# Kernel optimization log

Measured on AMD Instinct MI355X. Metric: run time of the kernel, lower is better.

## Reference

```python
import jax, jax.numpy as jnp
import numpy as np

B, NS, NQ = 128, 128, 512
D_IN, D_OUT = 256, 64


def setup_inputs() -> dict:
    key = jax.random.key(0)
    ks = jax.random.split(key, 6)
    return {
        "phi_support": jax.random.normal(ks[0], (B, NS, D_IN), dtype=jnp.float32),
        "y_support": jax.random.normal(ks[1], (B, NS, D_OUT), dtype=jnp.float32),
        "phi_query": jax.random.normal(ks[2], (B, NQ, D_IN), dtype=jnp.float32),
        "y_query": jax.random.normal(ks[3], (B, NQ, D_OUT), dtype=jnp.float32),
        # xavier-uniform-ish params
        "m_prior": jax.random.uniform(ks[4], (D_IN, D_OUT), minval=-1.0, maxval=1.0) * np.sqrt(6.0 / (D_IN + D_OUT)),
        "S_inv_prior_asym": jax.random.uniform(ks[5], (D_IN, D_IN), minval=-1.0, maxval=1.0) * np.sqrt(6.0 / (2 * D_IN)),
        "sig_eps": jnp.array([0.1], dtype=jnp.float32),
    }


def reference(phi_support, y_support, phi_query, y_query, m_prior, S_inv_prior_asym, sig_eps):
    alpha = 1.0
    d_out = m_prior.shape[1]
    # prior precision (symmetric PSD by construction) and natural-param prior mean
    S_inv_prior = alpha * (S_inv_prior_asym @ S_inv_prior_asym.T)          # [D_in, D_in]
    m_prior_nat = S_inv_prior @ m_prior                                     # [D_in, D_out]
    # posterior precision / covariance per task (nobs > 0 branch)
    S_inv = jnp.einsum('bni,bnj->bij', phi_support, phi_support) + S_inv_prior  # [B, D_in, D_in]
    S = jnp.linalg.inv(S_inv)                                               # batched small inverse
    rhs = jnp.einsum('bni,bnk->bik', phi_support, y_support) + m_prior_nat  # [B, D_in, D_out]
    m = S @ rhs                                                             # [B, D_in, D_out]
    # predictive mean and spread
    mu = phi_query @ m                                                      # [B, Q, D_out]
    spread_fac = 1.0 + jnp.einsum('bqi,bij,bqj->bq', phi_query, S, phi_query)  # [B, Q]
    # sig = spread_fac (x) (eye * sig_eps) : diagonal [B, Q, D_out, D_out]
    diag = jnp.eye(d_out, dtype=mu.dtype) * sig_eps                         # [D_out, D_out]
    sig = spread_fac[..., None, None] * diag
    # nll: logdet of diagonal sig + quadratic form with its inverse (diag -> reciprocal)
    logdet = d_out * (jnp.log(spread_fac) + jnp.log(sig_eps))               # [B, Q]
    resid = y_query - mu
    quadf = jnp.sum(resid * resid, axis=-1) / (spread_fac * sig_eps)        # [B, Q]
    nll = logdet.mean() + quadf.mean()
    return mu, sig, nll
```

## Files before the change

kernel.cpp:

```cpp
#include <hip/hip_runtime.h>
#include <math.h>

#define B_T   128
#define NS    128
#define NQ    512
#define DIN   256
#define DOUT  64

#define MU_SIZE  (B_T*NQ*DOUT)
#define SIG_SIZE (B_T*NQ*DOUT*DOUT)
#define NLL_IDX  (MU_SIZE + SIG_SIZE)

__global__ __launch_bounds__(256) void k_prior_sp(const float* __restrict__ A,
                                                  double* __restrict__ Sp,
                                                  double* __restrict__ NLLACC) {
    __shared__ float Ai[16][260];
    __shared__ float Aj[16][260];
    int bi = blockIdx.x;
    int i0 = (bi >> 4) << 4;
    int j0 = (bi & 15) << 4;
    int tid = threadIdx.x;
    if (bi == 0 && tid == 0) NLLACC[0] = 0.0;
    for (int idx = tid; idx < 16 * 256; idx += 256) {
        int r = idx >> 8, c = idx & 255;
        Ai[r][c] = A[(i0 + r) * 256 + c];
        Aj[r][c] = A[(j0 + r) * 256 + c];
    }
    __syncthreads();
    int r = tid >> 4, c = tid & 15;
    double acc = 0.0;
    for (int k = 0; k < 256; ++k)
        acc += (double)Ai[r][k] * (double)Aj[c][k];
    Sp[(i0 + r) * 256 + (j0 + c)] = acc;
}

__global__ __launch_bounds__(256) void k_build_G(const float* __restrict__ PHI,
                                                 const double* __restrict__ Sp,
                                                 double* __restrict__ G) {
    __shared__ float As[128][64];
    __shared__ float Bs[128][64];
    int b = blockIdx.x;
    int by = blockIdx.y;
    int ti = 0;
    while (((ti + 1) * (ti + 2)) / 2 <= by) ti++;
    int tj = by - (ti * (ti + 1)) / 2;
    int i0 = ti * 64, j0 = tj * 64;
    int tid = threadIdx.x;
    const float* Pb = PHI + b * (NS * DIN);
    for (int idx = tid; idx < 128 * 64; idx += 256) {
        int n = idx >> 6, c = idx & 63;
        As[n][c] = Pb[n * 256 + i0 + c];
        Bs[n][c] = Pb[n * 256 + j0 + c];
    }
    __syncthreads();
    int tx = tid & 15, ty = tid >> 4;
    double acc[4][4];
#pragma unroll
    for (int r = 0; r < 4; ++r)
#pragma unroll
        for (int s = 0; s < 4; ++s) acc[r][s] = 0.0;
    for (int n = 0; n < 128; ++n) {
        float a0 = As[n][4 * ty + 0], a1 = As[n][4 * ty + 1];
        float a2 = As[n][4 * ty + 2], a3 = As[n][4 * ty + 3];
        float b0 = Bs[n][4 * tx + 0], b1 = Bs[n][4 * tx + 1];
        float b2 = Bs[n][4 * tx + 2], b3 = Bs[n][4 * tx + 3];
        acc[0][0] += (double)a0 * b0; acc[0][1] += (double)a0 * b1;
        acc[0][2] += (double)a0 * b2; acc[0][3] += (double)a0 * b3;
        acc[1][0] += (double)a1 * b0; acc[1][1] += (double)a1 * b1;
        acc[1][2] += (double)a1 * b2; acc[1][3] += (double)a1 * b3;
        acc[2][0] += (double)a2 * b0; acc[2][1] += (double)a2 * b1;
        acc[2][2] += (double)a2 * b2; acc[2][3] += (double)a2 * b3;
        acc[3][0] += (double)a3 * b0; acc[3][1] += (double)a3 * b1;
        acc[3][2] += (double)a3 * b2; acc[3][3] += (double)a3 * b3;
    }
    double* Gb = G + b * 65536;
#pragma unroll
    for (int r = 0; r < 4; ++r) {
        int i = i0 + 4 * ty + r;
#pragma unroll
        for (int s = 0; s < 4; ++s) {
            int j = j0 + 4 * tx + s;
            Gb[i * 256 + j] = acc[r][s] + Sp[i * 256 + j];
        }
    }
}

__global__ __launch_bounds__(256) void k_build_rhs(const float* __restrict__ PHI,
                                                   const float* __restrict__ Y,
                                                   const float* __restrict__ MP,
                                                   const double* __restrict__ Sp,
                                                   double* __restrict__ RHS,
                                                   double* __restrict__ MPNo) {
    int b = blockIdx.x, by = blockIdx.y, tid = threadIdx.x;
    if (by == 4) {
        if (b >= 4) return;
        for (int out = tid; out < 4096; out += 256) {
            int r = 64 * b + (out >> 6), cc = out & 63;
            double acc = 0.0;
            for (int t = 0; t < 256; ++t)
                acc += Sp[r * 256 + t] * (double)MP[t * 64 + cc];
            MPNo[r * 64 + cc] = acc;
        }
        return;
    }
    __shared__ float As[128][64];
    __shared__ float Ys[128][64];
    int i0 = by * 64;
    const float* Pb = PHI + b * (NS * DIN);
    const float* Yb = Y + b * (NS * DOUT);
    for (int idx = tid; idx < 128 * 64; idx += 256) {
        int n = idx >> 6, c = idx & 63;
        As[n][c] = Pb[n * 256 + i0 + c];
        Ys[n][c] = Yb[n * 64 + c];
    }
    __syncthreads();
    int tx = tid & 15, ty = tid >> 4;
    double acc[4][4];
#pragma unroll
    for (int r = 0; r < 4; ++r)
#pragma unroll
        for (int s = 0; s < 4; ++s) acc[r][s] = 0.0;
    for (int n = 0; n < 128; ++n) {
        float a0 = As[n][4 * ty + 0], a1 = As[n][4 * ty + 1];
        float a2 = As[n][4 * ty + 2], a3 = As[n][4 * ty + 3];
        float y0 = Ys[n][4 * tx + 0], y1 = Ys[n][4 * tx + 1];
        float y2 = Ys[n][4 * tx + 2], y3 = Ys[n][4 * tx + 3];
        acc[0][0] += (double)a0 * y0; acc[0][1] += (double)a0 * y1;
        acc[0][2] += (double)a0 * y2; acc[0][3] += (double)a0 * y3;
        acc[1][0] += (double)a1 * y0; acc[1][1] += (double)a1 * y1;
        acc[1][2] += (double)a1 * y2; acc[1][3] += (double)a1 * y3;
        acc[2][0] += (double)a2 * y0; acc[2][1] += (double)a2 * y1;
        acc[2][2] += (double)a2 * y2; acc[2][3] += (double)a2 * y3;
        acc[3][0] += (double)a3 * y0; acc[3][1] += (double)a3 * y1;
        acc[3][2] += (double)a3 * y2; acc[3][3] += (double)a3 * y3;
    }
    double* Rb = RHS + b * 16384;
#pragma unroll
    for (int r = 0; r < 4; ++r) {
        int i = i0 + 4 * ty + r;
#pragma unroll
        for (int s = 0; s < 4; ++s)
            Rb[i * 64 + 4 * tx + s] = acc[r][s];
    }
}

__global__ __launch_bounds__(256) void k_cholinv(double* __restrict__ G,
                                                 double* __restrict__ LT,
                                                 double* __restrict__ TI,
                                                 float* __restrict__ TIF) {
    __shared__ double S[8256];
    int b = blockIdx.x, tid = threadIdx.x;
    double* Gb = G + b * 65536;
    double* LTb = LT + b * 65536;
    double* TIb = TI + b * 65536;
    float* TIFb = TIF + b * 65536;

    double* P = S;
#define PCH(p, r) P[(p) * 258 + (r)]
    for (int k0 = 0; k0 < 256; k0 += 32) {
        int rows = 256 - k0;
        for (int idx = tid; idx < rows * 32; idx += 256) {
            int r = k0 + (idx >> 5), p = idx & 31;
            PCH(p, r) = Gb[r * 256 + k0 + p];
        }
        __syncthreads();
        for (int p = 0; p < 32; ++p) {
            int k = k0 + p;
            if (tid >= k) {
                double v = PCH(p, tid);
                for (int p2 = 0; p2 < p; ++p2) v -= PCH(p2, tid) * PCH(p2, k);
                PCH(p, tid) = v;
            }
            __syncthreads();
            double d = sqrt(fmax(PCH(p, k), 1e-300));
            double inv = 1.0 / d;
            if (tid > k) PCH(p, tid) *= inv;
            else if (tid == k) PCH(p, tid) = d;
            __syncthreads();
        }
        for (int p = 0; p < 32; ++p) {
            int k = k0 + p;
            if (tid >= k) LTb[k * 256 + tid] = PCH(p, tid);
        }
        int ty = tid >> 4, tx = tid & 15;
        for (int i2 = k0 + 32 + 2 * ty; i2 < 256; i2 += 32) {
            double pa[32], pb[32];
#pragma unroll
            for (int p = 0; p < 32; ++p) { pa[p] = PCH(p, i2); pb[p] = PCH(p, i2 + 1); }
            for (int j2 = k0 + 32 + 2 * tx; j2 <= i2 + 1; j2 += 32) {
                double g00 = 0.0, g01 = 0.0, g10 = 0.0, g11 = 0.0;
#pragma unroll
                for (int p = 0; p < 32; ++p) {
                    double q0 = PCH(p, j2), q1 = PCH(p, j2 + 1);
                    g00 += pa[p] * q0; g01 += pa[p] * q1;
                    g10 += pb[p] * q0; g11 += pb[p] * q1;
                }
                if (j2 <= i2)     Gb[i2 * 256 + j2]           -= g00;
                if (j2 + 1 <= i2) Gb[i2 * 256 + j2 + 1]       -= g01;
                Gb[(i2 + 1) * 256 + j2] -= g10;
                if (j2 <= i2)     Gb[(i2 + 1) * 256 + j2 + 1] -= g11;
            }
        }
        __syncthreads();
    }
#undef PCH

    double* SHD = S;
    for (int idx = tid; idx < 65536; idx += 256) {
        int i = idx >> 8, k = idx & 255;
        if (k > i) { TIb[idx] = 0.0; TIFb[idx] = 0.0f; }
    }
    for (int idx = tid; idx < 8192; idx += 256) {
        int g = idx >> 10, rem = idx & 1023, k = rem >> 5, i = rem & 31;
        SHD[idx] = LTb[(32 * g + k) * 256 + 32 * g + i];
    }
    __syncthreads();
    {
        int g = tid >> 5, j = tid & 31;
        const double* D = SHD + g * 1024;
        double x[32];
#pragma unroll
        for (int i = 0; i < 32; ++i) {
            double s = (i == j) ? 1.0 : 0.0;
#pragma unroll
            for (int k = 0; k < i; ++k) {
                double lv = D[k * 32 + i];
                s -= (k >= j) ? lv * x[k] : 0.0;
            }
            double inv = 1.0 / D[i * 32 + i];
            x[i] = (i >= j) ? s * inv : 0.0;
        }
#pragma unroll
        for (int i = 0; i < 32; ++i) {
            int gi = 32 * g + i, gj = 32 * g + j;
            TIb[gi * 256 + gj] = x[i];
            TIFb[gi * 256 + gj] = (float)x[i];
        }
    }
    __syncthreads();
    double* Bsh = SHD;
    int j = tid & 31, ig = tid >> 5;
    for (int I = 1; I < 8; ++I) {
        for (int J = I - 1; J >= 0; --J) {
            double acc[4] = {0.0, 0.0, 0.0, 0.0};
            for (int K = J; K < I; ++K) {
                for (int kk = 0; kk < 32; ++kk) {
                    double tv = TIb[(32 * K + kk) * 256 + 32 * J + j];
#pragma unroll
                    for (int r = 0; r < 4; ++r) {
                        double lv = LTb[(32 * K + kk) * 256 + 32 * I + ig * 4 + r];
                        acc[r] += lv * tv;
                    }
                }
            }
            __syncthreads();
#pragma unroll
            for (int r = 0; r < 4; ++r) Bsh[(ig * 4 + r) * 32 + j] = acc[r];
            __syncthreads();
            double c[4] = {0.0, 0.0, 0.0, 0.0};
            for (int k = 0; k < 32; ++k) {
                double bv = Bsh[k * 32 + j];
#pragma unroll
                for (int r = 0; r < 4; ++r) {
                    double dv = TIb[(32 * I + ig * 4 + r) * 256 + 32 * I + k];
                    c[r] -= dv * bv;
                }
            }
#pragma unroll
            for (int r = 0; r < 4; ++r) {
                int gi = 32 * I + ig * 4 + r, gj = 32 * J + j;
                TIb[gi * 256 + gj] = c[r];
                TIFb[gi * 256 + gj] = (float)c[r];
            }
        }
        __syncthreads();
    }
}

__global__ __launch_bounds__(256) void k_gemm_Z(const double* __restrict__ TI,
                                                const double* __restrict__ RHS,
                                                const double* __restrict__ MPN,
                                                double* __restrict__ Z) {
    __shared__ double As[32][64];
    __shared__ double Bs[64][64];
    int b = blockIdx.x, i0 = blockIdx.y * 32;
    int tid = threadIdx.x, c = tid & 63, rg = tid >> 6;
    const double* TIb = TI + b * 65536;
    const double* Rb = RHS + b * 16384;
    double* Zb = Z + b * 16384;
    double acc[8] = {};
    for (int k0 = 0; k0 <= i0; k0 += 64) {
        for (int idx = tid; idx < 2048; idx += 256) {
            int r = idx >> 6, kk = idx & 63;
            As[r][kk] = TIb[(i0 + r) * 256 + k0 + kk];
        }
        for (int idx = tid; idx < 4096; idx += 256) {
            int kk = idx >> 6, cc = idx & 63;
            Bs[kk][cc] = Rb[(k0 + kk) * 64 + cc] + MPN[(k0 + kk) * 64 + cc];
        }
        __syncthreads();
        for (int kk = 0; kk < 64; ++kk) {
            double bv = Bs[kk][c];
#pragma unroll
            for (int r = 0; r < 8; ++r)
                acc[r] += As[rg * 8 + r][kk] * bv;
        }
        __syncthreads();
    }
#pragma unroll
    for (int r = 0; r < 8; ++r)
        Zb[(i0 + rg * 8 + r) * 64 + c] = acc[r];
}

__global__ __launch_bounds__(256) void k_gemm_M(const double* __restrict__ TI,
                                                const double* __restrict__ Z,
                                                double* __restrict__ M) {
    __shared__ double As[64][32];
    __shared__ double Bs[64][64];
    int b = blockIdx.x, i0 = blockIdx.y * 32;
    int tid = threadIdx.x, c = tid & 63, rg = tid >> 6;
    const double* TIb = TI + b * 65536;
    const double* Zb = Z + b * 16384;
    double* Mb = M + b * 16384;
    double acc[8] = {};
    for (int k0 = (i0 >> 6) << 6; k0 < 256; k0 += 64) {
        for (int idx = tid; idx < 2048; idx += 256) {
            int kk = idx >> 5, ri = idx & 31;
            As[kk][ri] = TIb[(k0 + kk) * 256 + i0 + ri];
        }
        for (int idx = tid; idx < 4096; idx += 256) {
            int kk = idx >> 6, cc = idx & 63;
            Bs[kk][cc] = Zb[(k0 + kk) * 64 + cc];
        }
        __syncthreads();
        for (int kk = 0; kk < 64; ++kk) {
            double bv = Bs[kk][c];
#pragma unroll
            for (int r = 0; r < 8; ++r)
                acc[r] += As[kk][rg * 8 + r] * bv;
        }
        __syncthreads();
    }
#pragma unroll
    for (int r = 0; r < 8; ++r)
        Mb[(i0 + rg * 8 + r) * 64 + c] = acc[r];
}

__global__ __launch_bounds__(256) void k_spread_gemm(const float* __restrict__ PHIQ,
                                                     const float* __restrict__ TIF,
                                                     float* __restrict__ PSUM) {
    __shared__ float Qs[64][65];
    __shared__ float Ts[64][65];
    int b = blockIdx.x, q0 = blockIdx.y * 64, I = blockIdx.z, i0 = I * 64;
    int tid = threadIdx.x, tx = tid & 15, ty = tid >> 4;
    const float* Qb = PHIQ + b * (NQ * DIN) + q0 * DIN;
    const float* Tb = TIF + b * 65536;
    float acc[4][4];
#pragma unroll
    for (int r = 0; r < 4; ++r)
#pragma unroll
        for (int s = 0; s < 4; ++s) acc[r][s] = 0.0f;
    for (int k0 = 0; k0 <= i0; k0 += 64) {
        for (int idx = tid; idx < 4096; idx += 256) {
            int r = idx >> 6, c = idx & 63;
            Qs[r][c] = Qb[r * 256 + k0 + c];
            Ts[c][r] = Tb[(i0 + r) * 256 + k0 + c];
        }
        __syncthreads();
        for (int kk = 0; kk < 64; ++kk) {
            float a0 = Qs[4 * ty + 0][kk], a1 = Qs[4 * ty + 1][kk];
            float a2 = Qs[4 * ty + 2][kk], a3 = Qs[4 * ty + 3][kk];
            float b0 = Ts[kk][4 * tx + 0], b1 = Ts[kk][4 * tx + 1];
            float b2 = Ts[kk][4 * tx + 2], b3 = Ts[kk][4 * tx + 3];
            acc[0][0] += a0 * b0; acc[0][1] += a0 * b1; acc[0][2] += a0 * b2; acc[0][3] += a0 * b3;
            acc[1][0] += a1 * b0; acc[1][1] += a1 * b1; acc[1][2] += a1 * b2; acc[1][3] += a1 * b3;
            acc[2][0] += a2 * b0; acc[2][1] += a2 * b1; acc[2][2] += a2 * b2; acc[2][3] += a2 * b3;
            acc[3][0] += a3 * b0; acc[3][1] += a3 * b1; acc[3][2] += a3 * b2; acc[3][3] += a3 * b3;
        }
        __syncthreads();
    }
#pragma unroll
    for (int r = 0; r < 4; ++r) {
        float p = acc[r][0] * acc[r][0] + acc[r][1] * acc[r][1]
                + acc[r][2] * acc[r][2] + acc[r][3] * acc[r][3];
        p += __shfl_down(p, 8, 16);
        p += __shfl_down(p, 4, 16);
        p += __shfl_down(p, 2, 16);
        p += __shfl_down(p, 1, 16);
        if (tx == 0) PSUM[(size_t)(b * 4 + I) * 512 + q0 + 4 * ty + r] = p;
    }
}

__global__ __launch_bounds__(256) void k_mu_nll(const float* __restrict__ PHIQ,
                                                const double* __restrict__ M,
                                                const float* __restrict__ YQ,
                                                const float* __restrict__ PSUM,
                                                const float* __restrict__ SE,
                                                float* __restrict__ SPREAD,
                                                double* __restrict__ NLLACC,
                                                float* __restrict__ MU) {
    __shared__ float Qs[64][65];
    __shared__ float Ms[64][64];
    __shared__ double nred[64];
    int b = blockIdx.x, q0 = blockIdx.y * 64, tid = threadIdx.x;
    int tx = tid & 15, ty = tid >> 4;
    const float* Qb = PHIQ + b * (NQ * DIN) + q0 * DIN;
    const double* Mb = M + b * 16384;
    float acc[4][4];
#pragma unroll
    for (int r = 0; r < 4; ++r)
#pragma unroll
        for (int s = 0; s < 4; ++s) acc[r][s] = 0.0f;
    for (int c0 = 0; c0 < 256; c0 += 64) {
        for (int idx = tid; idx < 4096; idx += 256) {
            int r = idx >> 6, c = idx & 63;
            Qs[r][c] = Qb[r * 256 + c0 + c];
            Ms[r][c] = (float)Mb[(c0 + r) * 64 + c];
        }
        __syncthreads();
        for (int kk = 0; kk < 64; ++kk) {
            float a0 = Qs[4 * ty + 0][kk], a1 = Qs[4 * ty + 1][kk];
            float a2 = Qs[4 * ty + 2][kk], a3 = Qs[4 * ty + 3][kk];
            float b0 = Ms[kk][4 * tx + 0], b1 = Ms[kk][4 * tx + 1];
            float b2 = Ms[kk][4 * tx + 2], b3 = Ms[kk][4 * tx + 3];
            acc[0][0] += a0 * b0; acc[0][1] += a0 * b1; acc[0][2] += a0 * b2; acc[0][3] += a0 * b3;
            acc[1][0] += a1 * b0; acc[1][1] += a1 * b1; acc[1][2] += a1 * b2; acc[1][3] += a1 * b3;
            acc[2][0] += a2 * b0; acc[2][1] += a2 * b1; acc[2][2] += a2 * b2; acc[2][3] += a2 * b3;
            acc[3][0] += a3 * b0; acc[3][1] += a3 * b1; acc[3][2] += a3 * b2; acc[3][3] += a3 * b3;
        }
        __syncthreads();
    }
    float se = SE[0];
#pragma unroll
    for (int r = 0; r < 4; ++r) {
        int q = q0 + 4 * ty + r;
        float4 v = make_float4(acc[r][0], acc[r][1], acc[r][2], acc[r][3]);
        *(float4*)&MU[((size_t)b * NQ + q) * 64 + 4 * tx] = v;
        float4 y = *(const float4*)&YQ[((size_t)b * NQ + q) * 64 + 4 * tx];
        float dx = y.x - v.x, dy = y.y - v.y, dz = y.z - v.z, dw = y.w - v.w;
        float qs = dx * dx + dy * dy + dz * dz + dw * dw;
        qs += __shfl_down(qs, 8, 16);
        qs += __shfl_down(qs, 4, 16);
        qs += __shfl_down(qs, 2, 16);
        qs += __shfl_down(qs, 1, 16);
        if (tx == 0) {
            float sp = 1.0f + PSUM[(size_t)(b * 4 + 0) * 512 + q]
                            + PSUM[(size_t)(b * 4 + 1) * 512 + q]
                            + PSUM[(size_t)(b * 4 + 2) * 512 + q]
                            + PSUM[(size_t)(b * 4 + 3) * 512 + q];
            SPREAD[b * 512 + q] = sp;
            float val = 64.0f * (logf(sp) + logf(se)) + qs / (sp * se);
            nred[ty * 4 + r] = (double)val;
        }
    }
    __syncthreads();
    for (int s = 32; s > 0; s >>= 1) {
        if (tid < s) nred[tid] += nred[tid + s];
        __syncthreads();
    }
    if (tid == 0) atomicAdd(NLLACC, nred[0] * (1.0 / 65536.0));
}

__global__ __launch_bounds__(256) void k_sig(const float* __restrict__ SPREAD,
                                             const float* __restrict__ SE,
                                             const double* __restrict__ NLLACC,
                                             float* __restrict__ out) {
    __shared__ float sv_s;
    int bq = blockIdx.x, tid = threadIdx.x;
    if (bq == 0 && tid == 0) out[NLL_IDX] = (float)NLLACC[0];
    if (tid == 0) sv_s = SPREAD[bq] * SE[0];
    __syncthreads();
    float sv = sv_s;
    float* base = out + (size_t)MU_SIZE + (size_t)bq * 4096;
    int i = tid >> 2;
    int jb = (tid & 3) << 4;
    int d = i - jb;
    float vals[16];
#pragma unroll
    for (int t = 0; t < 16; ++t) vals[t] = (t == d) ? sv : 0.0f;
    float4* p = (float4*)(base + tid * 16);
    p[0] = make_float4(vals[0], vals[1], vals[2], vals[3]);
    p[1] = make_float4(vals[4], vals[5], vals[6], vals[7]);
    p[2] = make_float4(vals[8], vals[9], vals[10], vals[11]);
    p[3] = make_float4(vals[12], vals[13], vals[14], vals[15]);
}

extern "C" void kernel_launch(void* const* d_in, const int* in_sizes, int n_in,
                              void* d_out, int out_size, void* d_ws, size_t ws_size,
                              hipStream_t stream) {
    const float* PHI_S = (const float*)d_in[0];
    const float* Y_S   = (const float*)d_in[1];
    const float* PHI_Q = (const float*)d_in[2];
    const float* Y_Q   = (const float*)d_in[3];
    const float* MP    = (const float*)d_in[4];
    const float* AP    = (const float*)d_in[5];
    const float* SE    = (const float*)d_in[6];
    float* out = (float*)d_out;

    double* scratch = (double*)(out + MU_SIZE);
    double* G    = scratch;
    double* LT   = G + 8388608;
    double* RHS  = LT + 8388608;
    double* Z    = RHS + 2097152;
    double* TI   = Z + 2097152;
    double* Spd  = TI + 8388608;
    double* MPN  = Spd + 65536;
    float*  TIF  = (float*)(MPN + 16384);
    float*  PSUM = TIF + 8388608;
    float*  SPREAD = (float*)d_ws;
    double* NLLACC = (double*)((char*)d_ws + 65536 * 4);

    k_prior_sp   <<<256, 256, 0, stream>>>(AP, Spd, NLLACC);
    k_build_G    <<<dim3(B_T, 10), 256, 0, stream>>>(PHI_S, Spd, G);
    k_build_rhs  <<<dim3(B_T, 5), 256, 0, stream>>>(PHI_S, Y_S, MP, Spd, RHS, MPN);
    k_cholinv    <<<B_T, 256, 0, stream>>>(G, LT, TI, TIF);
    k_gemm_Z     <<<dim3(B_T, 8), 256, 0, stream>>>(TI, RHS, MPN, Z);
    k_gemm_M     <<<dim3(B_T, 8), 256, 0, stream>>>(TI, Z, RHS);
    k_spread_gemm<<<dim3(B_T, 8, 4), 256, 0, stream>>>(PHI_Q, TIF, PSUM);
    k_mu_nll     <<<dim3(B_T, 8), 256, 0, stream>>>(PHI_Q, RHS, Y_Q, PSUM, SE,
                                                    SPREAD, NLLACC, out);
    k_sig        <<<65536, 256, 0, stream>>>(SPREAD, SE, NLLACC, out);
}
```

Baseline: 2.433 ms.

## Restructure batched Cholesky-inverse kernel with 1024 threads and warp-level panel factorization

The Cholesky/triangular-inverse kernel now runs 1024 threads per block instead of 256. Each 32-column diagonal panel is factored inside one wavefront using shuffles instead of block barriers. The rows below the panel are solved by a separate thread-per-row step, and the block-triangular inverse stage stages its L and TI tiles in shared memory with one output element per thread. The aim is to cut the serial barrier chain and idle threads in a kernel that only launches 128 blocks, at the cost of more syncthreads in the inverse loop and higher register pressure at 1024 threads.

```diff
diff --git a/kernel.cpp b/kernel.cpp
--- a/kernel.cpp
+++ b/kernel.cpp
@@ -144,11 +144,12 @@
     }
 }
 
-__global__ __launch_bounds__(256) void k_cholinv(double* __restrict__ G,
-                                                 double* __restrict__ LT,
-                                                 double* __restrict__ TI,
-                                                 float* __restrict__ TIF) {
+__global__ __launch_bounds__(1024) void k_cholinv(double* __restrict__ G,
+                                                  double* __restrict__ LT,
+                                                  double* __restrict__ TI,
+                                                  float* __restrict__ TIF) {
     __shared__ double S[8256];
+    __shared__ double dinvs[32];
     int b = blockIdx.x, tid = threadIdx.x;
     double* Gb = G + b * 65536;
     double* LTb = LT + b * 65536;
@@ -159,65 +160,82 @@
 #define PCH(p, r) P[(p) * 258 + (r)]
     for (int k0 = 0; k0 < 256; k0 += 32) {
         int rows = 256 - k0;
-        for (int idx = tid; idx < rows * 32; idx += 256) {
+        for (int idx = tid; idx < rows * 32; idx += 1024) {
             int r = k0 + (idx >> 5), p = idx & 31;
             PCH(p, r) = Gb[r * 256 + k0 + p];
         }
         __syncthreads();
-        for (int p = 0; p < 32; ++p) {
-            int k = k0 + p;
-            if (tid >= k) {
-                double v = PCH(p, tid);
-                for (int p2 = 0; p2 < p; ++p2) v -= PCH(p2, tid) * PCH(p2, k);
-                PCH(p, tid) = v;
+        if (tid < 32) {
+            double x[32];
+#pragma unroll
+            for (int p = 0; p < 32; ++p) x[p] = PCH(p, k0 + tid);
+            for (int p = 0; p < 32; ++p) {
+                double dpp = __shfl(x[p], p);
+                double d = sqrt(fmax(dpp, 1e-300));
+                double inv = 1.0 / d;
+                if (tid == p) { x[p] = d; dinvs[p] = inv; }
+                else if (tid > p) x[p] *= inv;
+                for (int p2 = p + 1; p2 < 32; ++p2) {
+                    double lp2 = __shfl(x[p], p2);
+                    if (tid >= p2) x[p2] -= x[p] * lp2;
+                }
             }
-            __syncthreads();
-            double d = sqrt(fmax(PCH(p, k), 1e-300));
-            double inv = 1.0 / d;
-            if (tid > k) PCH(p, tid) *= inv;
-            else if (tid == k) PCH(p, tid) = d;
-            __syncthreads();
-        }
-        for (int p = 0; p < 32; ++p) {
-            int k = k0 + p;
-            if (tid >= k) LTb[k * 256 + tid] = PCH(p, tid);
+#pragma unroll
+            for (int p = 0; p < 32; ++p) PCH(p, k0 + tid) = x[p];
+        }
+        __syncthreads();
+        {
+            int i = k0 + 32 + tid;
+            if (i < 256) {
+                double xr[32];
+#pragma unroll
+                for (int p = 0; p < 32; ++p) {
+                    double v = PCH(p, i);
+                    for (int p2 = 0; p2 < p; ++p2)
+                        v -= xr[p2] * PCH(p2, k0 + p);
+                    xr[p] = v * dinvs[p];
+                }
+#pragma unroll
+                for (int p = 0; p < 32; ++p) PCH(p, i) = xr[p];
+            }
+        }
+        __syncthreads();
+        for (int idx = tid; idx < 8192; idx += 1024) {
+            int p = idx >> 8, r = idx & 255;
+            if (r >= k0 + p) LTb[(k0 + p) * 256 + r] = PCH(p, r);
         }
         int ty = tid >> 4, tx = tid & 15;
-        for (int i2 = k0 + 32 + 2 * ty; i2 < 256; i2 += 32) {
-            double pa[32], pb[32];
-#pragma unroll
-            for (int p = 0; p < 32; ++p) { pa[p] = PCH(p, i2); pb[p] = PCH(p, i2 + 1); }
-            for (int j2 = k0 + 32 + 2 * tx; j2 <= i2 + 1; j2 += 32) {
-                double g00 = 0.0, g01 = 0.0, g10 = 0.0, g11 = 0.0;
+        for (int i2 = k0 + 32 + ty; i2 < 256; i2 += 64) {
+            double pa[32];
+#pragma unroll
+            for (int p = 0; p < 32; ++p) pa[p] = PCH(p, i2);
+            for (int j2 = k0 + 32 + 2 * tx; j2 <= i2; j2 += 32) {
+                double g0 = 0.0, g1 = 0.0;
 #pragma unroll
                 for (int p = 0; p < 32; ++p) {
-                    double q0 = PCH(p, j2), q1 = PCH(p, j2 + 1);
-                    g00 += pa[p] * q0; g01 += pa[p] * q1;
-                    g10 += pb[p] * q0; g11 += pb[p] * q1;
+                    g0 += pa[p] * PCH(p, j2);
+                    g1 += pa[p] * PCH(p, j2 + 1);
                 }
-                if (j2 <= i2)     Gb[i2 * 256 + j2]           -= g00;
-                if (j2 + 1 <= i2) Gb[i2 * 256 + j2 + 1]       -= g01;
-                Gb[(i2 + 1) * 256 + j2] -= g10;
-                if (j2 <= i2)     Gb[(i2 + 1) * 256 + j2 + 1] -= g11;
+                Gb[i2 * 256 + j2] -= g0;
+                if (j2 + 1 <= i2) Gb[i2 * 256 + j2 + 1] -= g1;
             }
         }
         __syncthreads();
     }
 #undef PCH
 
-    double* SHD = S;
-    for (int idx = tid; idx < 65536; idx += 256) {
+    for (int idx = tid; idx < 65536; idx += 1024) {
         int i = idx >> 8, k = idx & 255;
         if (k > i) { TIb[idx] = 0.0; TIFb[idx] = 0.0f; }
     }
-    for (int idx = tid; idx < 8192; idx += 256) {
+    for (int idx = tid; idx < 8192; idx += 1024) {
         int g = idx >> 10, rem = idx & 1023, k = rem >> 5, i = rem & 31;
-        SHD[idx] = LTb[(32 * g + k) * 256 + 32 * g + i];
-    }
-    __syncthreads();
-    {
+        S[idx] = LTb[(32 * g + k) * 256 + 32 * g + i];
+    }
+    __syncthreads();
+    if (tid < 256) {
         int g = tid >> 5, j = tid & 31;
-        const double* D = SHD + g * 1024;
+        const double* D = S + g * 1024;
         double x[32];
 #pragma unroll
         for (int i = 0; i < 32; ++i) {
@@ -227,8 +245,7 @@
                 double lv = D[k * 32 + i];
                 s -= (k >= j) ? lv * x[k] : 0.0;
             }
-            double inv = 1.0 / D[i * 32 + i];
-            x[i] = (i >= j) ? s * inv : 0.0;
+            x[i] = (i >= j) ? s * (1.0 / D[i * 32 + i]) : 0.0;
         }
 #pragma unroll
         for (int i = 0; i < 32; ++i) {
@@ -238,42 +255,39 @@
         }
     }
     __syncthreads();
-    double* Bsh = SHD;
-    int j = tid & 31, ig = tid >> 5;
+    double* Lsh = S;
+    double* Tsh = S + 1024;
+    double* Bsh = S + 2048;
+    double* Dsh = S + 3072;
+    int ei = tid >> 5, ej = tid & 31;
     for (int I = 1; I < 8; ++I) {
+        __syncthreads();
+        Dsh[tid] = TIb[(32 * I + ei) * 256 + 32 * I + ej];
+        __syncthreads();
         for (int J = I - 1; J >= 0; --J) {
-            double acc[4] = {0.0, 0.0, 0.0, 0.0};
+            double a = 0.0;
             for (int K = J; K < I; ++K) {
-                for (int kk = 0; kk < 32; ++kk) {
-                    double tv = TIb[(32 * K + kk) * 256 + 32 * J + j];
-#pragma unroll
-                    for (int r = 0; r < 4; ++r) {
-                        double lv = LTb[(32 * K + kk) * 256 + 32 * I + ig * 4 + r];
-                        acc[r] += lv * tv;
-                    }
+                __syncthreads();
+                {
+                    int kk = tid >> 5, e = tid & 31;
+                    Lsh[tid] = LTb[(32 * K + kk) * 256 + 32 * I + e];
+                    Tsh[tid] = TIb[(32 * K + kk) * 256 + 32 * J + e];
                 }
+                __syncthreads();
+#pragma unroll 8
+                for (int kk = 0; kk < 32; ++kk)
+                    a += Lsh[kk * 32 + ei] * Tsh[kk * 32 + ej];
             }
             __syncthreads();
-#pragma unroll
-            for (int r = 0; r < 4; ++r) Bsh[(ig * 4 + r) * 32 + j] = acc[r];
+            Bsh[tid] = a;
             __syncthreads();
-            double c[4] = {0.0, 0.0, 0.0, 0.0};
-            for (int k = 0; k < 32; ++k) {
-                double bv = Bsh[k * 32 + j];
-#pragma unroll
-                for (int r = 0; r < 4; ++r) {
-                    double dv = TIb[(32 * I + ig * 4 + r) * 256 + 32 * I + k];
-                    c[r] -= dv * bv;
-                }
-            }
-#pragma unroll
-            for (int r = 0; r < 4; ++r) {
-                int gi = 32 * I + ig * 4 + r, gj = 32 * J + j;
-                TIb[gi * 256 + gj] = c[r];
-                TIFb[gi * 256 + gj] = (float)c[r];
-            }
-        }
-        __syncthreads();
+            double c = 0.0;
+#pragma unroll 8
+            for (int kk = 0; kk < 32; ++kk)
+                c -= Dsh[ei * 32 + kk] * Bsh[kk * 32 + ej];
+            TIb[(32 * I + ei) * 256 + 32 * J + ej] = c;
+            TIFb[(32 * I + ei) * 256 + 32 * J + ej] = (float)c;
+        }
     }
 }
 
@@ -513,7 +527,7 @@
     k_prior_sp   <<<256, 256, 0, stream>>>(AP, Spd, NLLACC);
     k_build_G    <<<dim3(B_T, 10), 256, 0, stream>>>(PHI_S, Spd, G);
     k_build_rhs  <<<dim3(B_T, 5), 256, 0, stream>>>(PHI_S, Y_S, MP, Spd, RHS, MPN);
-    k_cholinv    <<<B_T, 256, 0, stream>>>(G, LT, TI, TIF);
+    k_cholinv    <<<B_T, 1024, 0, stream>>>(G, LT, TI, TIF);
     k_gemm_Z     <<<dim3(B_T, 8), 256, 0, stream>>>(TI, RHS, MPN, Z);
     k_gemm_M     <<<dim3(B_T, 8), 256, 0, stream>>>(TI, Z, RHS);
     k_spread_gemm<<<dim3(B_T, 8, 4), 256, 0, stream>>>(PHI_Q, TIF, PSUM);
```

After: 4.012 ms. +64.9%, slower.
